# Kernel optimization log

Measured on AMD Instinct MI355X. Metric: run time of the kernel, lower is better.

Reference implementation:

```python
import jax, jax.numpy as jnp
import numpy as np

HEADS = 8


def setup_inputs() -> dict:
    key = jax.random.key(0)
    ks = jax.random.split(key, 5)
    B, C, H, W = 4, 256, 48, 48
    x = jax.random.normal(ks[0], (B, C, H, W), dtype=jnp.float32)
    # 1x1 conv weights == channel matmul matrices
    w_qkv = jax.random.normal(ks[1], (3 * C, C), dtype=jnp.float32) * (C ** -0.5)
    b_qkv = jax.random.normal(ks[2], (3 * C,), dtype=jnp.float32) * 0.02
    w_proj = jax.random.normal(ks[3], (C, C), dtype=jnp.float32) * (C ** -0.5)
    b_proj = jax.random.normal(ks[4], (C,), dtype=jnp.float32) * 0.02
    return {"x": x, "w_qkv": w_qkv, "b_qkv": b_qkv, "w_proj": w_proj, "b_proj": b_proj}


def reference(x, w_qkv, b_qkv, w_proj, b_proj):
    B, C, H, W = x.shape
    heads = HEADS
    dh = C // heads
    HW = H * W
    scale = dh ** -0.5
    # qkv 1x1 conv: [B, 3C, H, W]
    qkv = jnp.einsum('bchw,oc->bohw', x, w_qkv) + b_qkv[None, :, None, None]
    # reshape(B,3,heads,dh,HW).transpose(-2,-1) -> [B,3,heads,HW,dh]
    qkv = qkv.reshape(B, 3, heads, dh, HW).transpose(0, 1, 2, 4, 3)
    q = qkv[:, 0] * scale  # [B,h,HW,dh]
    k = qkv[:, 1]
    v = qkv[:, 2]
    scores = jnp.einsum('bhnd,bhmd->bhnm', q, k)  # [B,h,HW,HW]
    scores = scores - jnp.max(scores, axis=-1, keepdims=True)
    exp_scores = jnp.exp(scores)
    weights = exp_scores / jnp.maximum(exp_scores.sum(axis=-1, keepdims=True), 1e-12)
    attn = jnp.einsum('bhnm,bhmd->bhnd', weights, v)  # [B,h,HW,dh]
    # transpose(2,3).reshape(B,C,H,W): [B,h,dh,HW] -> [B,C,H,W]
    attn = attn.transpose(0, 1, 3, 2).reshape(B, C, H, W)
    out = jnp.einsum('bchw,oc->bohw', attn, w_proj) + b_proj[None, :, None, None]
    return out
```

## Files before the change

### kernel.cpp

```cpp
#include <hip/hip_runtime.h>
#include <math.h>

#define HW 2304
#define QS 0.2550565355f

typedef _Float16 f16;
typedef __attribute__((ext_vector_type(4))) _Float16 f16x4;
typedef __attribute__((ext_vector_type(8))) _Float16 f16x8;
typedef __attribute__((ext_vector_type(4))) float f32x4;

#if __has_builtin(__builtin_amdgcn_exp2f)
#define EXP2F(x) __builtin_amdgcn_exp2f(x)
#else
#define EXP2F(x) exp2f(x)
#endif

static __device__ __forceinline__ f16x4 pack4(float a, float b, float c, float d) {
    auto lo = __builtin_amdgcn_cvt_pkrtz(a, b);
    auto hi = __builtin_amdgcn_cvt_pkrtz(c, d);
    f16x4 r;
    r[0] = (f16)lo[0]; r[1] = (f16)lo[1]; r[2] = (f16)hi[0]; r[3] = (f16)hi[1];
    return r;
}

__global__ __launch_bounds__(256) void cvt_w(const float* __restrict__ wq,
                                             const float* __restrict__ wp,
                                             f16* __restrict__ wh) {
    const int i = (blockIdx.x * 256 + threadIdx.x) * 4;
    float4 v;
    if (i < 768 * 256) v = *(const float4*)(wq + i);
    else               v = *(const float4*)(wp + (i - 768 * 256));
    f16x4 h = {(f16)v.x, (f16)v.y, (f16)v.z, (f16)v.w};
    *(f16x4*)(wh + i) = h;
}

__global__ __launch_bounds__(256) void cvt_x(const float* __restrict__ x,
                                             f16* __restrict__ xt) {
    __shared__ f16 tile[64][72];
    const int t  = threadIdx.x;
    const int n0 = blockIdx.x * 64, c0 = blockIdx.y * 64, b = blockIdx.z;
    const float* xb = x + ((size_t)b * 256 + c0) * HW + n0;
#pragma unroll
    for (int pass = 0; pass < 4; ++pass) {
        const int u  = t + pass * 256;
        const int cr = u >> 4, cc = u & 15;
        const float4 v = *(const float4*)(xb + (size_t)cr * HW + 4 * cc);
        tile[4 * cc + 0][cr] = (f16)v.x;
        tile[4 * cc + 1][cr] = (f16)v.y;
        tile[4 * cc + 2][cr] = (f16)v.z;
        tile[4 * cc + 3][cr] = (f16)v.w;
    }
    __syncthreads();
    f16* xo = xt + ((size_t)b * HW + n0) * 256 + c0;
#pragma unroll
    for (int pass = 0; pass < 2; ++pass) {
        const int u  = t + pass * 256;
        const int nr = u >> 3, nc = u & 7;
        *(f16x8*)(xo + (size_t)nr * 256 + 8 * nc) = *(const f16x8*)&tile[nr][8 * nc];
    }
}

__global__ __launch_bounds__(64) void qkv_gemm(const f16* __restrict__ xt,
                                               const f16* __restrict__ wh,
                                               const float* __restrict__ bias,
                                               f16* __restrict__ qt,
                                               f16* __restrict__ kt,
                                               f16* __restrict__ vn) {
    const int lane = threadIdx.x & 63;
    const int c    = lane & 15, q4 = lane >> 4;
    const int n0   = blockIdx.x * 64;
    const int m0   = blockIdx.y * 64;
    const int b    = blockIdx.z;
    const int s    = (blockIdx.x + blockIdx.y) & 7;
    const f16* xb  = xt + (size_t)b * HW * 256;

    f32x4 C[4][4] = {};
    f16x8 af[2][4], bf[2][4];
    const int k0 = s * 32;
#pragma unroll
    for (int mt = 0; mt < 4; ++mt)
        af[0][mt] = *(const f16x8*)(wh + (size_t)(m0 + mt * 16 + c) * 256 + k0 + q4 * 8);
#pragma unroll
    for (int nt = 0; nt < 4; ++nt)
        bf[0][nt] = *(const f16x8*)(xb + (size_t)(n0 + nt * 16 + c) * 256 + k0 + q4 * 8);

#pragma unroll
    for (int it = 0; it < 8; ++it) {
        const int p = it & 1, pn = p ^ 1;
        const int kn = ((s + it + 1) & 7) * 32;
#pragma unroll
        for (int mt = 0; mt < 4; ++mt)
            af[pn][mt] = *(const f16x8*)(wh + (size_t)(m0 + mt * 16 + c) * 256 + kn + q4 * 8);
#pragma unroll
        for (int nt = 0; nt < 4; ++nt)
            bf[pn][nt] = *(const f16x8*)(xb + (size_t)(n0 + nt * 16 + c) * 256 + kn + q4 * 8);
#pragma unroll
        for (int mt = 0; mt < 4; ++mt)
#pragma unroll
            for (int nt = 0; nt < 4; ++nt)
                C[mt][nt] = __builtin_amdgcn_mfma_f32_16x16x32_f16(af[p][mt], bf[p][nt], C[mt][nt], 0, 0, 0);
    }

#pragma unroll
    for (int mt = 0; mt < 4; ++mt) {
        const int od = m0 + mt * 16 + q4 * 4;
        const float4 bv = *(const float4*)(bias + od);
        const int seg = od >> 8;
        const int oo  = od & 255;
        const int h   = oo >> 5, d0 = oo & 31;
        const size_t bh = (size_t)b * 8 + h;
#pragma unroll
        for (int nt = 0; nt < 4; ++nt) {
            const int n = n0 + nt * 16 + c;
            float v0 = C[mt][nt][0] + bv.x;
            float v1 = C[mt][nt][1] + bv.y;
            float v2 = C[mt][nt][2] + bv.z;
            float v3 = C[mt][nt][3] + bv.w;
            if (seg == 0) {
                v0 *= QS; v1 *= QS; v2 *= QS; v3 *= QS;
                f16x4 hv = {(f16)v0, (f16)v1, (f16)v2, (f16)v3};
                *(f16x4*)(qt + (bh * HW + n) * 32 + d0) = hv;
            } else if (seg == 1) {
                f16x4 hv = {(f16)v0, (f16)v1, (f16)v2, (f16)v3};
                *(f16x4*)(kt + (bh * HW + n) * 32 + d0) = hv;
            } else {
                const int nsw = n0 + (c >> 2) * 16 + nt * 4 + (c & 3);
                vn[(bh * 32 + d0 + 0) * HW + nsw] = (f16)v0;
                vn[(bh * 32 + d0 + 1) * HW + nsw] = (f16)v1;
                vn[(bh * 32 + d0 + 2) * HW + nsw] = (f16)v2;
                vn[(bh * 32 + d0 + 3) * HW + nsw] = (f16)v3;
            }
        }
    }
}

__global__ __launch_bounds__(256, 3) void attn_kernel(const f16* __restrict__ qt,
                                                      const f16* __restrict__ kt,
                                                      const f16* __restrict__ vn,
                                                      f16* __restrict__ at) {
    __shared__ float ored[2][96][36];
    __shared__ float lred[2][96];

    const int t    = threadIdx.x;
    const int lane = t & 63;
    const int w    = t >> 6;
    const int gh   = w >> 1;
    const int jh   = w & 1;
    const int c    = lane & 15, q4 = lane >> 4;
    const int bhid = blockIdx.x;
    const int h    = bhid & 7, b = bhid >> 3;
    const int i0   = blockIdx.y * 96;
    const size_t bh = (size_t)b * 8 + h;

    const f16* qtb = qt + bh * (size_t)HW * 32;
    const f16* kb = kt + bh * (size_t)HW * 32 + (size_t)(jh * 1152 + c) * 32 + q4 * 8;
    const f16* vb = vn + bh * (size_t)32 * HW + (size_t)c * HW + jh * 1152 + q4 * 16;

    f16x8 qf[3];
#pragma unroll
    for (int g = 0; g < 3; ++g)
        qf[g] = *(const f16x8*)(qtb + (size_t)(i0 + gh * 48 + g * 16 + c) * 32 + q4 * 8);

    const f16 oneh = (f16)(c == 0 ? 1.0f : 0.0f);
    const f16x4 ones = {oneh, oneh, oneh, oneh};

    f32x4 O[3][2] = {};
    f32x4 lacc[3] = {};

    f16x8 kA[4], kB[4];
    f16x4 vA[2][4], vB[2][4];

#define LOADK(dst, j) {                                                        \
        const f16* p_ = kb + (size_t)(j) * 32;                                 \
        dst[0] = *(const f16x8*)(p_);                                          \
        dst[1] = *(const f16x8*)(p_ + 512);                                    \
        dst[2] = *(const f16x8*)(p_ + 1024);                                   \
        dst[3] = *(const f16x8*)(p_ + 1536);                                   \
    }
#define LOADV(dst, j) {                                                        \
        const f16* p_ = vb + (j);                                              \
        *(f16x8*)&dst[0][0] = *(const f16x8*)(p_);                             \
        *(f16x8*)&dst[0][2] = *(const f16x8*)(p_ + 8);                         \
        *(f16x8*)&dst[1][0] = *(const f16x8*)(p_ + 16 * HW);                   \
        *(f16x8*)&dst[1][2] = *(const f16x8*)(p_ + 16 * HW + 8);               \
    }
#define COMPUTE(kf, vv) {                                                      \
        const f32x4 z_ = {0.f, 0.f, 0.f, 0.f};                                 \
        _Pragma("unroll")                                                      \
        for (int t4 = 0; t4 < 4; ++t4) {                                       \
            f16x4 P[3];                                                        \
            _Pragma("unroll")                                                  \
            for (int g = 0; g < 3; ++g) {                                      \
                const f32x4 S = __builtin_amdgcn_mfma_f32_16x16x32_f16(        \
                    kf[t4], qf[g], z_, 0, 0, 0);                               \
                P[g] = pack4(EXP2F(S[0]), EXP2F(S[1]), EXP2F(S[2]),            \
                             EXP2F(S[3]));                                     \
            }                                                                  \
            _Pragma("unroll")                                                  \
            for (int g = 0; g < 3; ++g) {                                      \
                O[g][0] = __builtin_amdgcn_mfma_f32_16x16x16f16(               \
                    vv[0][t4], P[g], O[g][0], 0, 0, 0);                        \
                O[g][1] = __builtin_amdgcn_mfma_f32_16x16x16f16(               \
                    vv[1][t4], P[g], O[g][1], 0, 0, 0);                        \
                lacc[g] = __builtin_amdgcn_mfma_f32_16x16x16f16(               \
                    ones, P[g], lacc[g], 0, 0, 0);                             \
            }                                                                  \
        }                                                                      \
    }

    LOADK(kA, 0);
    LOADV(vA, 0);
#pragma unroll 1
    for (int s = 0; s < 9; ++s) {
        const int j1 = s * 128 + 64;
        const int j2 = (s == 8) ? 0 : j1 + 64;
        LOADK(kB, j1);
        LOADV(vB, j1);
        COMPUTE(kA, vA);
        LOADK(kA, j2);
        LOADV(vA, j2);
        COMPUTE(kB, vB);
    }
#undef LOADK
#undef LOADV
#undef COMPUTE

#pragma unroll
    for (int g = 0; g < 3; ++g) {
        const int row = gh * 48 + g * 16 + c;
#pragma unroll
        for (int dh = 0; dh < 2; ++dh)
            *(f32x4*)&ored[jh][row][dh * 16 + q4 * 4] = O[g][dh];
        if (q4 == 0) lred[jh][row] = lacc[g][0];
    }
    __syncthreads();

    if (t < 192) {
        const int i   = t >> 1;
        const int d16 = (t & 1) * 16;
        const float l = lred[0][i] + lred[1][i];
        const float inv = 1.f / fmaxf(l, 1e-12f);
        float4 s[4];
#pragma unroll
        for (int k = 0; k < 4; ++k) {
            const float4 pa = *(const float4*)&ored[0][i][d16 + 4 * k];
            const float4 pb = *(const float4*)&ored[1][i][d16 + 4 * k];
            s[k].x = pa.x + pb.x; s[k].y = pa.y + pb.y;
            s[k].z = pa.z + pb.z; s[k].w = pa.w + pb.w;
        }
        f16* op = at + ((size_t)b * HW + i0 + i) * 256 + h * 32 + d16;
        *(f16x4*)(op + 0)  = pack4(s[0].x * inv, s[0].y * inv, s[0].z * inv, s[0].w * inv);
        *(f16x4*)(op + 4)  = pack4(s[1].x * inv, s[1].y * inv, s[1].z * inv, s[1].w * inv);
        *(f16x4*)(op + 8)  = pack4(s[2].x * inv, s[2].y * inv, s[2].z * inv, s[2].w * inv);
        *(f16x4*)(op + 12) = pack4(s[3].x * inv, s[3].y * inv, s[3].z * inv, s[3].w * inv);
    }
}

__global__ __launch_bounds__(64) void proj_gemm(const f16* __restrict__ at,
                                                const f16* __restrict__ wh,
                                                const float* __restrict__ bias,
                                                float* __restrict__ out) {
    const int lane = threadIdx.x & 63;
    const int c    = lane & 15, q4 = lane >> 4;
    const int n0   = blockIdx.x * 64;
    const int m0   = blockIdx.y * 64;
    const int b    = blockIdx.z;
    const int s    = (blockIdx.x + blockIdx.y) & 7;
    const f16* ab  = at + (size_t)b * HW * 256;

    f32x4 C[4][4] = {};
    f16x8 af[2][4], bf[2][4];
    const int k0 = s * 32;
#pragma unroll
    for (int mt = 0; mt < 4; ++mt)
        af[0][mt] = *(const f16x8*)(wh + (size_t)(m0 + mt * 16 + c) * 256 + k0 + q4 * 8);
#pragma unroll
    for (int nt = 0; nt < 4; ++nt)
        bf[0][nt] = *(const f16x8*)(ab + (size_t)(n0 + nt * 16 + c) * 256 + k0 + q4 * 8);

#pragma unroll
    for (int it = 0; it < 8; ++it) {
        const int p = it & 1, pn = p ^ 1;
        const int kn = ((s + it + 1) & 7) * 32;
#pragma unroll
        for (int mt = 0; mt < 4; ++mt)
            af[pn][mt] = *(const f16x8*)(wh + (size_t)(m0 + mt * 16 + c) * 256 + kn + q4 * 8);
#pragma unroll
        for (int nt = 0; nt < 4; ++nt)
            bf[pn][nt] = *(const f16x8*)(ab + (size_t)(n0 + nt * 16 + c) * 256 + kn + q4 * 8);
#pragma unroll
        for (int mt = 0; mt < 4; ++mt)
#pragma unroll
            for (int nt = 0; nt < 4; ++nt)
                C[mt][nt] = __builtin_amdgcn_mfma_f32_16x16x32_f16(af[p][mt], bf[p][nt], C[mt][nt], 0, 0, 0);
    }

#pragma unroll
    for (int mt = 0; mt < 4; ++mt) {
        const int od = m0 + mt * 16 + q4 * 4;
        const float4 bv = *(const float4*)(bias + od);
#pragma unroll
        for (int nt = 0; nt < 4; ++nt) {
            const int n = n0 + nt * 16 + c;
            out[((size_t)b * 256 + od + 0) * HW + n] = C[mt][nt][0] + bv.x;
            out[((size_t)b * 256 + od + 1) * HW + n] = C[mt][nt][1] + bv.y;
            out[((size_t)b * 256 + od + 2) * HW + n] = C[mt][nt][2] + bv.z;
            out[((size_t)b * 256 + od + 3) * HW + n] = C[mt][nt][3] + bv.w;
        }
    }
}

extern "C" void kernel_launch(void* const* d_in, const int* in_sizes, int n_in,
                              void* d_out, int out_size, void* d_ws, size_t ws_size,
                              hipStream_t stream) {
    const float* x      = (const float*)d_in[0];
    const float* w_qkv  = (const float*)d_in[1];
    const float* b_qkv  = (const float*)d_in[2];
    const float* w_proj = (const float*)d_in[3];
    const float* b_proj = (const float*)d_in[4];
    float* out = (float*)d_out;

    const size_t per = (size_t)4 * HW * 256;
    f16* xt = (f16*)d_ws;
    f16* wh = xt + per;
    f16* qt = wh + 262144;
    f16* kt = qt + per;
    f16* vn = kt + per;
    f16* at = vn + per;

    cvt_w<<<256, 256, 0, stream>>>(w_qkv, w_proj, wh);
    cvt_x<<<dim3(36, 4, 4), 256, 0, stream>>>(x, xt);
    qkv_gemm<<<dim3(36, 12, 4), 64, 0, stream>>>(xt, wh, b_qkv, qt, kt, vn);
    attn_kernel<<<dim3(32, 24), 256, 0, stream>>>(qt, kt, vn, at);
    proj_gemm<<<dim3(36, 4, 4), 64, 0, stream>>>(at, wh + 768 * 256, b_proj, out);
}
```

Before: 144.0 us.

## Merge conversion kernels, halve GEMM M-tiles, batch attention score MFMAs before exp

Merges the weight and activation fp16 conversion kernels into a single launch to save one kernel launch. Halves the M tile of the QKV and projection GEMMs from 64 to 32 rows, doubling the grid to give more blocks and better CU coverage, at the cost of less operand reuse per block. Reorders the attention inner COMPUTE so all 12 score MFMAs issue first, then all exps, then the PV MFMAs, which exposes more independent work to the scheduler but raises register pressure.

```diff
diff --git a/kernel.cpp b/kernel.cpp
--- a/kernel.cpp
+++ b/kernel.cpp
@@ -23,22 +23,26 @@
     return r;
 }
 
-__global__ __launch_bounds__(256) void cvt_w(const float* __restrict__ wq,
-                                             const float* __restrict__ wp,
-                                             f16* __restrict__ wh) {
-    const int i = (blockIdx.x * 256 + threadIdx.x) * 4;
-    float4 v;
-    if (i < 768 * 256) v = *(const float4*)(wq + i);
-    else               v = *(const float4*)(wp + (i - 768 * 256));
-    f16x4 h = {(f16)v.x, (f16)v.y, (f16)v.z, (f16)v.w};
-    *(f16x4*)(wh + i) = h;
-}
-
-__global__ __launch_bounds__(256) void cvt_x(const float* __restrict__ x,
-                                             f16* __restrict__ xt) {
+__global__ __launch_bounds__(256) void cvt_all(const float* __restrict__ x,
+                                               const float* __restrict__ wq,
+                                               const float* __restrict__ wp,
+                                               f16* __restrict__ xt,
+                                               f16* __restrict__ wh) {
     __shared__ f16 tile[64][72];
-    const int t  = threadIdx.x;
-    const int n0 = blockIdx.x * 64, c0 = blockIdx.y * 64, b = blockIdx.z;
+    const int bid = blockIdx.x;
+    const int t   = threadIdx.x;
+    if (bid >= 576) {
+        const int i = ((bid - 576) * 256 + t) * 4;
+        float4 v;
+        if (i < 768 * 256) v = *(const float4*)(wq + i);
+        else               v = *(const float4*)(wp + (i - 768 * 256));
+        f16x4 h = {(f16)v.x, (f16)v.y, (f16)v.z, (f16)v.w};
+        *(f16x4*)(wh + i) = h;
+        return;
+    }
+    const int bx = bid % 36, rem = bid / 36;
+    const int by = rem & 3, bz = rem >> 2;
+    const int n0 = bx * 64, c0 = by * 64, b = bz;
     const float* xb = x + ((size_t)b * 256 + c0) * HW + n0;
 #pragma unroll
     for (int pass = 0; pass < 4; ++pass) {
@@ -69,16 +73,16 @@
     const int lane = threadIdx.x & 63;
     const int c    = lane & 15, q4 = lane >> 4;
     const int n0   = blockIdx.x * 64;
-    const int m0   = blockIdx.y * 64;
+    const int m0   = blockIdx.y * 32;
     const int b    = blockIdx.z;
     const int s    = (blockIdx.x + blockIdx.y) & 7;
     const f16* xb  = xt + (size_t)b * HW * 256;
 
-    f32x4 C[4][4] = {};
-    f16x8 af[2][4], bf[2][4];
+    f32x4 C[2][4] = {};
+    f16x8 af[2][2], bf[2][4];
     const int k0 = s * 32;
 #pragma unroll
-    for (int mt = 0; mt < 4; ++mt)
+    for (int mt = 0; mt < 2; ++mt)
         af[0][mt] = *(const f16x8*)(wh + (size_t)(m0 + mt * 16 + c) * 256 + k0 + q4 * 8);
 #pragma unroll
     for (int nt = 0; nt < 4; ++nt)
@@ -89,20 +93,20 @@
         const int p = it & 1, pn = p ^ 1;
         const int kn = ((s + it + 1) & 7) * 32;
 #pragma unroll
-        for (int mt = 0; mt < 4; ++mt)
+        for (int mt = 0; mt < 2; ++mt)
             af[pn][mt] = *(const f16x8*)(wh + (size_t)(m0 + mt * 16 + c) * 256 + kn + q4 * 8);
 #pragma unroll
         for (int nt = 0; nt < 4; ++nt)
             bf[pn][nt] = *(const f16x8*)(xb + (size_t)(n0 + nt * 16 + c) * 256 + kn + q4 * 8);
 #pragma unroll
-        for (int mt = 0; mt < 4; ++mt)
+        for (int mt = 0; mt < 2; ++mt)
 #pragma unroll
             for (int nt = 0; nt < 4; ++nt)
                 C[mt][nt] = __builtin_amdgcn_mfma_f32_16x16x32_f16(af[p][mt], bf[p][nt], C[mt][nt], 0, 0, 0);
     }
 
 #pragma unroll
-    for (int mt = 0; mt < 4; ++mt) {
+    for (int mt = 0; mt < 2; ++mt) {
         const int od = m0 + mt * 16 + q4 * 4;
         const float4 bv = *(const float4*)(bias + od);
         const int seg = od >> 8;
@@ -186,26 +190,31 @@
     }
 #define COMPUTE(kf, vv) {                                                      \
         const f32x4 z_ = {0.f, 0.f, 0.f, 0.f};                                 \
+        f32x4 S[4][3];                                                         \
         _Pragma("unroll")                                                      \
-        for (int t4 = 0; t4 < 4; ++t4) {                                       \
-            f16x4 P[3];                                                        \
+        for (int t4 = 0; t4 < 4; ++t4)                                         \
             _Pragma("unroll")                                                  \
-            for (int g = 0; g < 3; ++g) {                                      \
-                const f32x4 S = __builtin_amdgcn_mfma_f32_16x16x32_f16(        \
+            for (int g = 0; g < 3; ++g)                                        \
+                S[t4][g] = __builtin_amdgcn_mfma_f32_16x16x32_f16(             \
                     kf[t4], qf[g], z_, 0, 0, 0);                               \
-                P[g] = pack4(EXP2F(S[0]), EXP2F(S[1]), EXP2F(S[2]),            \
-                             EXP2F(S[3]));                                     \
-            }                                                                  \
+        f16x4 P[4][3];                                                         \
+        _Pragma("unroll")                                                      \
+        for (int t4 = 0; t4 < 4; ++t4)                                         \
+            _Pragma("unroll")                                                  \
+            for (int g = 0; g < 3; ++g)                                        \
+                P[t4][g] = pack4(EXP2F(S[t4][g][0]), EXP2F(S[t4][g][1]),       \
+                                 EXP2F(S[t4][g][2]), EXP2F(S[t4][g][3]));      \
+        _Pragma("unroll")                                                      \
+        for (int t4 = 0; t4 < 4; ++t4)                                         \
             _Pragma("unroll")                                                  \
             for (int g = 0; g < 3; ++g) {                                      \
                 O[g][0] = __builtin_amdgcn_mfma_f32_16x16x16f16(               \
-                    vv[0][t4], P[g], O[g][0], 0, 0, 0);                        \
+                    vv[0][t4], P[t4][g], O[g][0], 0, 0, 0);                    \
                 O[g][1] = __builtin_amdgcn_mfma_f32_16x16x16f16(               \
-                    vv[1][t4], P[g], O[g][1], 0, 0, 0);                        \
+                    vv[1][t4], P[t4][g], O[g][1], 0, 0, 0);                    \
                 lacc[g] = __builtin_amdgcn_mfma_f32_16x16x16f16(               \
-                    ones, P[g], lacc[g], 0, 0, 0);                             \
+                    ones, P[t4][g], lacc[g], 0, 0, 0);                         \
             }                                                                  \
-        }                                                                      \
     }
 
     LOADK(kA, 0);
@@ -263,16 +272,16 @@
     const int lane = threadIdx.x & 63;
     const int c    = lane & 15, q4 = lane >> 4;
     const int n0   = blockIdx.x * 64;
-    const int m0   = blockIdx.y * 64;
+    const int m0   = blockIdx.y * 32;
     const int b    = blockIdx.z;
     const int s    = (blockIdx.x + blockIdx.y) & 7;
     const f16* ab  = at + (size_t)b * HW * 256;
 
-    f32x4 C[4][4] = {};
-    f16x8 af[2][4], bf[2][4];
+    f32x4 C[2][4] = {};
+    f16x8 af[2][2], bf[2][4];
     const int k0 = s * 32;
 #pragma unroll
-    for (int mt = 0; mt < 4; ++mt)
+    for (int mt = 0; mt < 2; ++mt)
         af[0][mt] = *(const f16x8*)(wh + (size_t)(m0 + mt * 16 + c) * 256 + k0 + q4 * 8);
 #pragma unroll
     for (int nt = 0; nt < 4; ++nt)
@@ -283,20 +292,20 @@
         const int p = it & 1, pn = p ^ 1;
         const int kn = ((s + it + 1) & 7) * 32;
 #pragma unroll
-        for (int mt = 0; mt < 4; ++mt)
+        for (int mt = 0; mt < 2; ++mt)
             af[pn][mt] = *(const f16x8*)(wh + (size_t)(m0 + mt * 16 + c) * 256 + kn + q4 * 8);
 #pragma unroll
         for (int nt = 0; nt < 4; ++nt)
             bf[pn][nt] = *(const f16x8*)(ab + (size_t)(n0 + nt * 16 + c) * 256 + kn + q4 * 8);
 #pragma unroll
-        for (int mt = 0; mt < 4; ++mt)
+        for (int mt = 0; mt < 2; ++mt)
 #pragma unroll
             for (int nt = 0; nt < 4; ++nt)
                 C[mt][nt] = __builtin_amdgcn_mfma_f32_16x16x32_f16(af[p][mt], bf[p][nt], C[mt][nt], 0, 0, 0);
     }
 
 #pragma unroll
-    for (int mt = 0; mt < 4; ++mt) {
+    for (int mt = 0; mt < 2; ++mt) {
         const int od = m0 + mt * 16 + q4 * 4;
         const float4 bv = *(const float4*)(bias + od);
 #pragma unroll
@@ -328,9 +337,8 @@
     f16* vn = kt + per;
     f16* at = vn + per;
 
-    cvt_w<<<256, 256, 0, stream>>>(w_qkv, w_proj, wh);
-    cvt_x<<<dim3(36, 4, 4), 256, 0, stream>>>(x, xt);
-    qkv_gemm<<<dim3(36, 12, 4), 64, 0, stream>>>(xt, wh, b_qkv, qt, kt, vn);
+    cvt_all<<<832, 256, 0, stream>>>(x, w_qkv, w_proj, xt, wh);
+    qkv_gemm<<<dim3(36, 24, 4), 64, 0, stream>>>(xt, wh, b_qkv, qt, kt, vn);
     attn_kernel<<<dim3(32, 24), 256, 0, stream>>>(qt, kt, vn, at);
-    proj_gemm<<<dim3(36, 4, 4), 64, 0, stream>>>(at, wh + 768 * 256, b_proj, out);
-}
+    proj_gemm<<<dim3(36, 8, 4), 64, 0, stream>>>(at, wh + 768 * 256, b_proj, out);
+}
```

Measured after the change: 148.2 us. +2.9%, slower.
